# Optimization experiments

Hardware: AMD Instinct MI355X
Metric: run time of the kernel (lower is better)

## Reference

```python
import jax, jax.numpy as jnp
import numpy as np

EPS = 1e-12  # matches torch F.normalize eps


def _l2n(x, axis):
    return x / jnp.maximum(jnp.linalg.norm(x, axis=axis, keepdims=True), EPS)


def setup_inputs() -> dict:
    key = jax.random.key(0)
    k1, k2, k3 = jax.random.split(key, 3)
    x = jax.random.normal(k1, (4, 128, 30, 40), dtype=jnp.float32)
    conv_w = jax.random.normal(k2, (64, 128), dtype=jnp.float32) * 0.02  # 1x1 conv, no bias (vladv2=False)
    centroids = jax.random.uniform(k3, (64, 128), dtype=jnp.float32)
    return {"x": x, "conv_w": conv_w, "centroids": centroids}


def reference(x, conv_w, centroids):
    N, C, H, W = x.shape
    K = centroids.shape[0]
    ps, stride = 4, 1  # patch_sizes='4', strides='1'

    # descriptor-wise L2 normalization of input
    x = _l2n(x, 1)

    # 1x1 conv + softmax over clusters -> soft assignment [N,K,H,W]
    soft_assign = jax.nn.softmax(jnp.einsum('kc,nchw->nkhw', conv_w, x), axis=1)

    # weighted residuals [N,K,C,H,W] (vectorized form of the per-cluster loop)
    res = (x[:, None] - centroids[None, :, :, None, None]) * soft_assign[:, :, None]

    # global VLAD: sum over spatial, intra-norm, flatten, L2-norm
    vlad_global = res.sum(axis=(-1, -2))            # [N,K,C]
    vlad_global = _l2n(vlad_global, 2).reshape(N, K * C)
    vlad_global = _l2n(vlad_global, 1)

    # integral image over spatial dims with zero pad on top/left
    r = res.reshape(N, K * C, H, W)
    integ = jnp.cumsum(jnp.cumsum(r, axis=-1), axis=-2)
    integ = jnp.pad(integ, ((0, 0), (0, 0), (1, 0), (1, 0)))  # [N,KC,H+1,W+1]

    # dilated 2x2 box-filter conv == 4-corner integral-image lookup
    TL = integ[:, :, :H + 1 - ps:stride, :W + 1 - ps:stride]
    TR = integ[:, :, :H + 1 - ps:stride, ps::stride]
    BL = integ[:, :, ps::stride, :W + 1 - ps:stride]
    BR = integ[:, :, ps::stride, ps::stride]
    vl = (TL - TR - BL + BR) / (ps * ps)            # [N,KC,Hp,Wp]
    Hp, Wp = vl.shape[-2], vl.shape[-1]

    # local VLAD: intra-norm over descriptor dim, then global L2 per patch
    vl = vl.reshape(N, K, C, Hp * Wp)
    vl = _l2n(vl, 2).reshape(N, K * C, Hp * Wp)
    vlad_local = _l2n(vl, 1)

    return vlad_global, vlad_local
```

## Files before the change

kernel.cpp:

```cpp
#include <hip/hip_runtime.h>
#include <math.h>

#define EPSV 1e-12f

namespace {
constexpr int N_  = 4;
constexpr int C_  = 128;
constexpr int H_  = 30;
constexpr int W_  = 40;
constexpr int K_  = 64;
constexpr int HW_ = H_ * W_;
constexpr int HP_ = 27;
constexpr int WP_ = 37;
constexpr int P_  = HP_ * WP_;
constexpr int KC_ = K_ * C_;
constexpr int CP_ = C_ * P_;
constexpr int CS_ = HP_ * W_;
constexpr int SL_ = CS_ / 4;
}

static __device__ __forceinline__ float4 ld4(const float* p) {
    return *reinterpret_cast<const float4*>(p);
}

__global__ __launch_bounds__(256) void k1_norm_softmax(
    const float* __restrict__ x, const float* __restrict__ conv_w,
    float* __restrict__ xnT, float* __restrict__ xnP, float* __restrict__ sa)
{
    __shared__ float xrow[C_ * W_];
    __shared__ float conv_s[K_ * C_];
    __shared__ float invn[W_];
    __shared__ float s_s[K_ * W_];

    const int b = blockIdx.x;
    const int n = b / H_, h = b - n * H_;
    const int t = threadIdx.x;

    for (int i = t; i < C_ * W_; i += 256) {
        const int c = i / W_, w = i - c * W_;
        xrow[i] = x[(size_t)(n * C_ + c) * HW_ + h * W_ + w];
    }
    for (int i = t; i < K_ * C_; i += 256) conv_s[i] = conv_w[i];
    __syncthreads();

    if (t < W_) {
        float s = 0.f;
        for (int c = 0; c < C_; ++c) { const float v = xrow[c * W_ + t]; s += v * v; }
        invn[t] = 1.f / fmaxf(sqrtf(s), EPSV);
    }
    __syncthreads();

    for (int i = t; i < C_ * W_; i += 256) {
        const int c = i / W_, w = i - c * W_;
        const float v = xrow[i] * invn[w];
        xrow[i] = v;
        xnT[(size_t)(n * C_ + c) * HW_ + h * W_ + w] = v;
    }
    __syncthreads();

    for (int i = t; i < W_ * C_; i += 256) {
        const int w = i / C_, c = i - w * C_;
        xnP[((size_t)n * HW_ + h * W_ + w) * C_ + c] = xrow[c * W_ + w];
    }

    for (int d = t; d < K_ * W_; d += 256) {
        const int k = d / W_, w = d - k * W_;
        const float* cw = &conv_s[k * C_];
        float s = 0.f;
        for (int c = 0; c < C_; ++c) s += cw[c] * xrow[c * W_ + w];
        s_s[d] = s;
    }
    __syncthreads();

    if (t < W_) {
        const int w = t;
        float m = -1e30f;
        for (int k = 0; k < K_; ++k) m = fmaxf(m, s_s[k * W_ + w]);
        float sum = 0.f;
        for (int k = 0; k < K_; ++k) sum += expf(s_s[k * W_ + w] - m);
        const float inv = 1.f / sum;
        for (int k = 0; k < K_; ++k)
            sa[(size_t)(n * K_ + k) * HW_ + h * W_ + w] = expf(s_s[k * W_ + w] - m) * inv;
    }
}

__global__ __launch_bounds__(256) void k2_vg(
    const float* __restrict__ sa, const float* __restrict__ xnP,
    const float* __restrict__ cent, float* __restrict__ vg_u,
    float* __restrict__ vg_r)
{
    const int b = blockIdx.x;
    const int n = b >> 6, k = b & 63;
    const int t = threadIdx.x;
    const int c = t & 127, half = t >> 7;
    constexpr int HHW = HW_ / 2;

    const float* sarow = &sa[(size_t)b * HW_ + half * HHW];
    const float* xp = &xnP[((size_t)n * HW_ + half * HHW) * C_ + c];
    float g0 = 0.f, g1 = 0.f, g2 = 0.f, g3 = 0.f;
    float b0 = 0.f, b1 = 0.f, b2 = 0.f, b3 = 0.f;
    for (int pix = 0; pix < HHW; pix += 4) {
        const float s0 = sarow[pix + 0], s1 = sarow[pix + 1];
        const float s2 = sarow[pix + 2], s3 = sarow[pix + 3];
        g0 += s0 * xp[(size_t)(pix + 0) * C_];
        g1 += s1 * xp[(size_t)(pix + 1) * C_];
        g2 += s2 * xp[(size_t)(pix + 2) * C_];
        g3 += s3 * xp[(size_t)(pix + 3) * C_];
        b0 += s0; b1 += s1; b2 += s2; b3 += s3;
    }
    const float g  = (g0 + g1) + (g2 + g3);
    const float bs = (b0 + b1) + (b2 + b3);

    __shared__ float gs[256], bss[256];
    __shared__ float red[2];
    gs[t] = g; bss[t] = bs;
    __syncthreads();

    float vg = 0.f;
    if (t < 128) {
        vg = (gs[t] + gs[t + 128]) - cent[k * C_ + c] * (bss[t] + bss[t + 128]);
        float nsq = vg * vg;
        for (int off = 32; off >= 1; off >>= 1) nsq += __shfl_down(nsq, off);
        if ((t & 63) == 0) red[t >> 6] = nsq;
    }
    __syncthreads();
    const float tot  = red[0] + red[1];
    const float norm = sqrtf(tot);
    const float iv   = 1.f / fmaxf(norm, EPSV);
    if (t < 128) vg_u[(size_t)b * C_ + t] = vg * iv;
    if (t == 0) { const float rr = norm * iv; vg_r[b] = rr * rr; }
}

__global__ __launch_bounds__(256) void k3_vg_fin(
    const float* __restrict__ vg_u, const float* __restrict__ vg_r,
    float* __restrict__ out)
{
    const int n = blockIdx.x;
    const int t = threadIdx.x;
    __shared__ float inv2s;
    if (t == 0) {
        float s = 0.f;
        for (int k = 0; k < K_; ++k) s += vg_r[n * K_ + k];
        inv2s = 1.f / fmaxf(sqrtf(s), EPSV);
    }
    __syncthreads();
    const float inv2 = inv2s;
    for (int i = t; i < KC_; i += 256)
        out[(size_t)n * KC_ + i] = vg_u[(size_t)n * KC_ + i] * inv2;
}

#define COLSUM_VEC(cs_s, sa_s, x0, x1, x2, x3)                                  \
    for (int s = t; s < SL_; s += 256) {                                        \
        const int i = s * 4;                                                    \
        const float4 sa0 = ld4(&sa_s[i]);                                       \
        const float4 sa1 = ld4(&sa_s[i + W_]);                                  \
        const float4 sa2 = ld4(&sa_s[i + 2 * W_]);                              \
        const float4 sa3 = ld4(&sa_s[i + 3 * W_]);                              \
        float acc[4][4];                                                        \
        const float* xc[4] = {x0, x1, x2, x3};                                  \
        _Pragma("unroll")                                                       \
        for (int ch = 0; ch < 4; ++ch) {                                        \
            const float4 a0 = ld4(xc[ch] + i);                                  \
            const float4 a1 = ld4(xc[ch] + i + W_);                             \
            const float4 a2 = ld4(xc[ch] + i + 2 * W_);                         \
            const float4 a3 = ld4(xc[ch] + i + 3 * W_);                         \
            acc[0][ch] = sa0.x * a0.x + sa1.x * a1.x + sa2.x * a2.x + sa3.x * a3.x; \
            acc[1][ch] = sa0.y * a0.y + sa1.y * a1.y + sa2.y * a2.y + sa3.y * a3.y; \
            acc[2][ch] = sa0.z * a0.z + sa1.z * a1.z + sa2.z * a2.z + sa3.z * a3.z; \
            acc[3][ch] = sa0.w * a0.w + sa1.w * a1.w + sa2.w * a2.w + sa3.w * a3.w; \
        }                                                                       \
        _Pragma("unroll")                                                       \
        for (int q = 0; q < 4; ++q)                                             \
            cs_s[i + q] = make_float4(acc[q][0], acc[q][1], acc[q][2], acc[q][3]); \
    }

__global__ __launch_bounds__(256) void k4_norm(
    const float* __restrict__ sa, const float* __restrict__ xnT,
    const float* __restrict__ cent, float* __restrict__ nsqp)
{
    __shared__ float  sa_s[HW_];
    __shared__ float  B_s[P_];
    __shared__ float4 cs_s[CS_];

    const int b  = blockIdx.x;
    const int cq = b & 3;
    const int nk = b >> 2;
    const int n  = nk >> 6, k = nk & 63;
    const int t  = threadIdx.x;

    for (int i = t; i < HW_; i += 256) sa_s[i] = sa[(size_t)nk * HW_ + i];
    __syncthreads();
    for (int p = t; p < P_; p += 256) {
        const int hp = p / WP_, wp = p - hp * WP_;
        float bs = 0.f;
#pragma unroll
        for (int dh = 0; dh < 4; ++dh) {
            const float* r = &sa_s[(hp + dh) * W_ + wp];
            bs += r[0] + r[1] + r[2] + r[3];
        }
        B_s[p] = bs;
    }

    float nsq0 = 0.f, nsq1 = 0.f, nsq2 = 0.f, nsq3 = 0.f;
    const float* xb = xnT + (size_t)n * C_ * HW_;

    for (int g = 0; g < 8; ++g) {
        const int c0 = cq * 32 + g * 4;
        const float* x0 = xb + (size_t)(c0 + 0) * HW_;
        const float* x1 = xb + (size_t)(c0 + 1) * HW_;
        const float* x2 = xb + (size_t)(c0 + 2) * HW_;
        const float* x3 = xb + (size_t)(c0 + 3) * HW_;
        __syncthreads();
        COLSUM_VEC(cs_s, sa_s, x0, x1, x2, x3)
        __syncthreads();
        const float4 ce = ld4(&cent[k * C_ + c0]);
#pragma unroll
        for (int pi = 0; pi < 4; ++pi) {
            const int p = t + pi * 256;
            if (p < P_) {
                const int hp = p / WP_, wp = p - hp * WP_;
                const int base = hp * W_ + wp;
                const float4 s0 = cs_s[base], s1 = cs_s[base + 1],
                             s2 = cs_s[base + 2], s3 = cs_s[base + 3];
                const float Bv = B_s[p];
                const float ux = (s0.x + s1.x + s2.x + s3.x) - ce.x * Bv;
                const float uy = (s0.y + s1.y + s2.y + s3.y) - ce.y * Bv;
                const float uz = (s0.z + s1.z + s2.z + s3.z) - ce.z * Bv;
                const float uw = (s0.w + s1.w + s2.w + s3.w) - ce.w * Bv;
                const float add = ux * ux + uy * uy + uz * uz + uw * uw;
                if      (pi == 0) nsq0 += add;
                else if (pi == 1) nsq1 += add;
                else if (pi == 2) nsq2 += add;
                else              nsq3 += add;
            }
        }
    }
#pragma unroll
    for (int pi = 0; pi < 4; ++pi) {
        const int p = t + pi * 256;
        if (p < P_) {
            const float v = (pi == 0 ? nsq0 : pi == 1 ? nsq1 : pi == 2 ? nsq2 : nsq3);
            nsqp[(size_t)b * P_ + p] = v * 0.00390625f;
        }
    }
}

__global__ __launch_bounds__(256) void k5_combine(
    const float* __restrict__ nsqp, float* __restrict__ inv1,
    float* __restrict__ rloc)
{
    const int nk = blockIdx.x;
    const int t  = threadIdx.x;
    for (int p = t; p < P_; p += 256) {
        const float s = nsqp[(size_t)(nk * 4 + 0) * P_ + p]
                      + nsqp[(size_t)(nk * 4 + 1) * P_ + p]
                      + nsqp[(size_t)(nk * 4 + 2) * P_ + p]
                      + nsqp[(size_t)(nk * 4 + 3) * P_ + p];
        const float norm = sqrtf(s);
        const float iv = 1.f / fmaxf(norm, EPSV);
        inv1[(size_t)nk * P_ + p] = iv * 0.0625f;
        const float rr = norm * iv;
        rloc[(size_t)nk * P_ + p] = rr * rr;
    }
}

__global__ __launch_bounds__(256) void k6_inv2(
    const float* __restrict__ rloc, float* __restrict__ inv2)
{
    const int n = blockIdx.x >> 2;
    const int p = (blockIdx.x & 3) * 256 + threadIdx.x;
    if (p < P_) {
        float s = 0.f;
        for (int k = 0; k < K_; ++k) s += rloc[(size_t)(n * K_ + k) * P_ + p];
        inv2[n * P_ + p] = 1.f / fmaxf(sqrtf(s), EPSV);
    }
}

__global__ __launch_bounds__(256) void k7_write(
    const float* __restrict__ sa, const float* __restrict__ xnT,
    const float* __restrict__ cent, const float* __restrict__ inv1,
    const float* __restrict__ inv2, float* __restrict__ outl)
{
    __shared__ float  sa_s[HW_];
    __shared__ float  scl_s[P_];
    __shared__ float  t2_s[P_];
    __shared__ float4 cs_s[CS_];

    const int b  = blockIdx.x;
    const int cq = b & 3;
    const int nk = b >> 2;
    const int n  = nk >> 6, k = nk & 63;
    const int t  = threadIdx.x;

    for (int i = t; i < HW_; i += 256) sa_s[i] = sa[(size_t)nk * HW_ + i];
    __syncthreads();
    for (int p = t; p < P_; p += 256) {
        const int hp = p / WP_, wp = p - hp * WP_;
        float bs = 0.f;
#pragma unroll
        for (int dh = 0; dh < 4; ++dh) {
            const float* r = &sa_s[(hp + dh) * W_ + wp];
            bs += r[0] + r[1] + r[2] + r[3];
        }
        const float sc = inv1[(size_t)nk * P_ + p] * inv2[n * P_ + p];
        scl_s[p] = sc;
        t2_s[p]  = bs * sc;
    }

    const float* xb = xnT + (size_t)n * C_ * HW_;
    float* ob = outl + (size_t)nk * CP_;

    for (int g = 0; g < 8; ++g) {
        const int c0 = cq * 32 + g * 4;
        const float* x0 = xb + (size_t)(c0 + 0) * HW_;
        const float* x1 = xb + (size_t)(c0 + 1) * HW_;
        const float* x2 = xb + (size_t)(c0 + 2) * HW_;
        const float* x3 = xb + (size_t)(c0 + 3) * HW_;
        __syncthreads();
        COLSUM_VEC(cs_s, sa_s, x0, x1, x2, x3)
        __syncthreads();
        const float4 ce = ld4(&cent[k * C_ + c0]);
#pragma unroll
        for (int pi = 0; pi < 4; ++pi) {
            const int p = t + pi * 256;
            if (p < P_) {
                const int hp = p / WP_, wp = p - hp * WP_;
                const int base = hp * W_ + wp;
                const float4 s0 = cs_s[base], s1 = cs_s[base + 1],
                             s2 = cs_s[base + 2], s3 = cs_s[base + 3];
                const float sc = scl_s[p];
                const float tt = t2_s[p];
                ob[(size_t)(c0 + 0) * P_ + p] = (s0.x + s1.x + s2.x + s3.x) * sc - ce.x * tt;
                ob[(size_t)(c0 + 1) * P_ + p] = (s0.y + s1.y + s2.y + s3.y) * sc - ce.y * tt;
                ob[(size_t)(c0 + 2) * P_ + p] = (s0.z + s1.z + s2.z + s3.z) * sc - ce.z * tt;
                ob[(size_t)(c0 + 3) * P_ + p] = (s0.w + s1.w + s2.w + s3.w) * sc - ce.w * tt;
            }
        }
    }
}

extern "C" void kernel_launch(void* const* d_in, const int* in_sizes, int n_in,
                              void* d_out, int out_size, void* d_ws, size_t ws_size,
                              hipStream_t stream)
{
    const float* x      = (const float*)d_in[0];
    const float* conv_w = (const float*)d_in[1];
    const float* cent   = (const float*)d_in[2];
    float* out = (float*)d_out;
    float* ws  = (float*)d_ws;

    float* xnT  = ws;
    float* xnP  = ws + 614400;
    float* sa   = ws + 1228800;
    float* vg_u = ws + 1536000;
    float* vg_r = ws + 1568768;
    float* nsqp = ws + 1569024;
    float* inv1 = ws + 2592000;
    float* rloc = ws + 2847744;
    float* inv2 = ws + 3103488;

    float* outl = out + (size_t)N_ * KC_;

    k1_norm_softmax<<<N_ * H_, 256, 0, stream>>>(x, conv_w, xnT, xnP, sa);
    k2_vg<<<N_ * K_, 256, 0, stream>>>(sa, xnP, cent, vg_u, vg_r);
    k3_vg_fin<<<N_, 256, 0, stream>>>(vg_u, vg_r, out);
    k4_norm<<<N_ * K_ * 4, 256, 0, stream>>>(sa, xnT, cent, nsqp);
    k5_combine<<<N_ * K_, 256, 0, stream>>>(nsqp, inv1, rloc);
    k6_inv2<<<N_ * 4, 256, 0, stream>>>(rloc, inv2);
    k7_write<<<N_ * K_ * 4, 256, 0, stream>>>(sa, xnT, cent, inv1, inv2, outl);
}
```

Baseline: 129.9 us.

## Widen k2 to 1024 threads and de-conflict column-sum LDS layout

k2_vg now splits the spatial reduction across eight thread groups in 1024-thread blocks instead of two groups of 128, raising parallelism for the 256-block launch. In k4_norm and k7_write, the shared column-sum buffer becomes four strided planes indexed by element mod 4, so consecutive writes from a thread and the shifted base+1..3 reads map to different banks. The aim is to cut LDS bank conflicts and k2 latency. The cost is a slightly more complex index calculation and a larger block with more shared-memory reduction work.

Result: faster. 126.1 us (-2.9%).

```diff
diff --git a/kernel.cpp b/kernel.cpp
--- a/kernel.cpp
+++ b/kernel.cpp
@@ -84,7 +84,7 @@
     }
 }
 
-__global__ __launch_bounds__(256) void k2_vg(
+__global__ __launch_bounds__(1024) void k2_vg(
     const float* __restrict__ sa, const float* __restrict__ xnP,
     const float* __restrict__ cent, float* __restrict__ vg_u,
     float* __restrict__ vg_r)
@@ -92,33 +92,32 @@
     const int b = blockIdx.x;
     const int n = b >> 6, k = b & 63;
     const int t = threadIdx.x;
-    const int c = t & 127, half = t >> 7;
-    constexpr int HHW = HW_ / 2;
-
-    const float* sarow = &sa[(size_t)b * HW_ + half * HHW];
-    const float* xp = &xnP[((size_t)n * HW_ + half * HHW) * C_ + c];
-    float g0 = 0.f, g1 = 0.f, g2 = 0.f, g3 = 0.f;
-    float b0 = 0.f, b1 = 0.f, b2 = 0.f, b3 = 0.f;
-    for (int pix = 0; pix < HHW; pix += 4) {
+    const int c = t & 127, eighth = t >> 7;
+    constexpr int CHW = HW_ / 8;
+
+    const float* sarow = &sa[(size_t)b * HW_ + eighth * CHW];
+    const float* xp = &xnP[((size_t)n * HW_ + eighth * CHW) * C_ + c];
+    float g0 = 0.f, g1 = 0.f, b0 = 0.f, b1 = 0.f;
+    for (int pix = 0; pix < CHW; pix += 2) {
         const float s0 = sarow[pix + 0], s1 = sarow[pix + 1];
-        const float s2 = sarow[pix + 2], s3 = sarow[pix + 3];
         g0 += s0 * xp[(size_t)(pix + 0) * C_];
         g1 += s1 * xp[(size_t)(pix + 1) * C_];
-        g2 += s2 * xp[(size_t)(pix + 2) * C_];
-        g3 += s3 * xp[(size_t)(pix + 3) * C_];
-        b0 += s0; b1 += s1; b2 += s2; b3 += s3;
-    }
-    const float g  = (g0 + g1) + (g2 + g3);
-    const float bs = (b0 + b1) + (b2 + b3);
-
-    __shared__ float gs[256], bss[256];
+        b0 += s0; b1 += s1;
+    }
+    const float g  = g0 + g1;
+    const float bs = b0 + b1;
+
+    __shared__ float gs[1024], bss[1024];
     __shared__ float red[2];
     gs[t] = g; bss[t] = bs;
     __syncthreads();
 
     float vg = 0.f;
     if (t < 128) {
-        vg = (gs[t] + gs[t + 128]) - cent[k * C_ + c] * (bss[t] + bss[t + 128]);
+        float gt = 0.f, bt = 0.f;
+#pragma unroll
+        for (int e = 0; e < 8; ++e) { gt += gs[t + 128 * e]; bt += bss[t + 128 * e]; }
+        vg = gt - cent[k * C_ + t] * bt;
         float nsq = vg * vg;
         for (int off = 32; off >= 1; off >>= 1) nsq += __shfl_down(nsq, off);
         if ((t & 63) == 0) red[t >> 6] = nsq;
@@ -149,7 +148,7 @@
         out[(size_t)n * KC_ + i] = vg_u[(size_t)n * KC_ + i] * inv2;
 }
 
-#define COLSUM_VEC(cs_s, sa_s, x0, x1, x2, x3)                                  \
+#define COLSUM_VEC_T(cs_q, sa_s, x0, x1, x2, x3)                                \
     for (int s = t; s < SL_; s += 256) {                                        \
         const int i = s * 4;                                                    \
         const float4 sa0 = ld4(&sa_s[i]);                                       \
@@ -171,8 +170,12 @@
         }                                                                       \
         _Pragma("unroll")                                                       \
         for (int q = 0; q < 4; ++q)                                             \
-            cs_s[i + q] = make_float4(acc[q][0], acc[q][1], acc[q][2], acc[q][3]); \
-    }
+            cs_q[q][s] = make_float4(acc[q][0], acc[q][1], acc[q][2], acc[q][3]); \
+    }
+
+static __device__ __forceinline__ float4 csget(const float4 cs_q[4][SL_], int e) {
+    return cs_q[e & 3][e >> 2];
+}
 
 __global__ __launch_bounds__(256) void k4_norm(
     const float* __restrict__ sa, const float* __restrict__ xnT,
@@ -180,7 +183,7 @@
 {
     __shared__ float  sa_s[HW_];
     __shared__ float  B_s[P_];
-    __shared__ float4 cs_s[CS_];
+    __shared__ float4 cs_q[4][SL_];
 
     const int b  = blockIdx.x;
     const int cq = b & 3;
@@ -211,7 +214,7 @@
         const float* x2 = xb + (size_t)(c0 + 2) * HW_;
         const float* x3 = xb + (size_t)(c0 + 3) * HW_;
         __syncthreads();
-        COLSUM_VEC(cs_s, sa_s, x0, x1, x2, x3)
+        COLSUM_VEC_T(cs_q, sa_s, x0, x1, x2, x3)
         __syncthreads();
         const float4 ce = ld4(&cent[k * C_ + c0]);
 #pragma unroll
@@ -220,8 +223,10 @@
             if (p < P_) {
                 const int hp = p / WP_, wp = p - hp * WP_;
                 const int base = hp * W_ + wp;
-                const float4 s0 = cs_s[base], s1 = cs_s[base + 1],
-                             s2 = cs_s[base + 2], s3 = cs_s[base + 3];
+                const float4 s0 = csget(cs_q, base);
+                const float4 s1 = csget(cs_q, base + 1);
+                const float4 s2 = csget(cs_q, base + 2);
+                const float4 s3 = csget(cs_q, base + 3);
                 const float Bv = B_s[p];
                 const float ux = (s0.x + s1.x + s2.x + s3.x) - ce.x * Bv;
                 const float uy = (s0.y + s1.y + s2.y + s3.y) - ce.y * Bv;
@@ -284,7 +289,7 @@
     __shared__ float  sa_s[HW_];
     __shared__ float  scl_s[P_];
     __shared__ float  t2_s[P_];
-    __shared__ float4 cs_s[CS_];
+    __shared__ float4 cs_q[4][SL_];
 
     const int b  = blockIdx.x;
     const int cq = b & 3;
@@ -317,7 +322,7 @@
         const float* x2 = xb + (size_t)(c0 + 2) * HW_;
         const float* x3 = xb + (size_t)(c0 + 3) * HW_;
         __syncthreads();
-        COLSUM_VEC(cs_s, sa_s, x0, x1, x2, x3)
+        COLSUM_VEC_T(cs_q, sa_s, x0, x1, x2, x3)
         __syncthreads();
         const float4 ce = ld4(&cent[k * C_ + c0]);
 #pragma unroll
@@ -326,8 +331,10 @@
             if (p < P_) {
                 const int hp = p / WP_, wp = p - hp * WP_;
                 const int base = hp * W_ + wp;
-                const float4 s0 = cs_s[base], s1 = cs_s[base + 1],
-                             s2 = cs_s[base + 2], s3 = cs_s[base + 3];
+                const float4 s0 = csget(cs_q, base);
+                const float4 s1 = csget(cs_q, base + 1);
+                const float4 s2 = csget(cs_q, base + 2);
+                const float4 s3 = csget(cs_q, base + 3);
                 const float sc = scl_s[p];
                 const float tt = t2_s[p];
                 ob[(size_t)(c0 + 0) * P_ + p] = (s0.x + s1.x + s2.x + s3.x) * sc - ce.x * tt;
@@ -362,7 +369,7 @@
     float* outl = out + (size_t)N_ * KC_;
 
     k1_norm_softmax<<<N_ * H_, 256, 0, stream>>>(x, conv_w, xnT, xnP, sa);
-    k2_vg<<<N_ * K_, 256, 0, stream>>>(sa, xnP, cent, vg_u, vg_r);
+    k2_vg<<<N_ * K_, 1024, 0, stream>>>(sa, xnP, cent, vg_u, vg_r);
     k3_vg_fin<<<N_, 256, 0, stream>>>(vg_u, vg_r, out);
     k4_norm<<<N_ * K_ * 4, 256, 0, stream>>>(sa, xnT, cent, nsqp);
     k5_combine<<<N_ * K_, 256, 0, stream>>>(nsqp, inv1, rloc);
```
